# Performance work log

Measured on AMD Instinct MI355X. Metric: run time of the kernel, lower is better.

Reference implementation:

```python
import jax, jax.numpy as jnp
import numpy as np

N, E, H = 100000, 600000, 128
N_MP = 4      # n_mp_down[0]
LN_EPS = 1e-5

def _ln(v, g, b):
    mu = jnp.mean(v, axis=-1, keepdims=True)
    var = jnp.mean((v - mu) ** 2, axis=-1, keepdims=True)
    return (v - mu) * jax.lax.rsqrt(var + LN_EPS) * g + b

def setup_inputs() -> dict:
    key = jax.random.key(0)
    ks = jax.random.split(key, 16)
    s = lambda fan_in: 1.0 / np.sqrt(fan_in)
    inp = {
        "x": jax.random.normal(ks[0], (N, H), jnp.float32),
        "edge_index": jax.random.randint(ks[1], (2, E), 0, N, jnp.int64),
        "edge_attr": jax.random.normal(ks[2], (E, H), jnp.float32),
        "pos": jax.random.uniform(ks[3], (N, 2), jnp.float32),
        "batch": jnp.zeros((N,), jnp.int64),
        # stacked per-iteration params (n_mlp_mp = 2 layers per MLP)
        "edge_w0": jax.random.uniform(ks[4], (N_MP, 3 * H, H), jnp.float32, -s(3 * H), s(3 * H)),
        "edge_b0": jnp.zeros((N_MP, H), jnp.float32),
        "edge_w1": jax.random.uniform(ks[5], (N_MP, H, H), jnp.float32, -s(H), s(H)),
        "edge_b1": jnp.zeros((N_MP, H), jnp.float32),
        "edge_ln_g": jnp.ones((N_MP, H), jnp.float32),
        "edge_ln_b": jnp.zeros((N_MP, H), jnp.float32),
        "node_w0": jax.random.uniform(ks[6], (N_MP, 2 * H, H), jnp.float32, -s(2 * H), s(2 * H)),
        "node_b0": jnp.zeros((N_MP, H), jnp.float32),
        "node_w1": jax.random.uniform(ks[7], (N_MP, H, H), jnp.float32, -s(H), s(H)),
        "node_b1": jnp.zeros((N_MP, H), jnp.float32),
        "node_ln_g": jnp.ones((N_MP, H), jnp.float32),
        "node_ln_b": jnp.zeros((N_MP, H), jnp.float32),
    }
    return inp

def reference(x, edge_index, edge_attr, pos, batch,
              edge_w0, edge_b0, edge_w1, edge_b1, edge_ln_g, edge_ln_b,
              node_w0, node_b0, node_w1, node_b1, node_ln_g, node_ln_b):
    src = edge_index[0]
    tgt = edge_index[1]
    n = x.shape[0]
    # degree for scatter-mean (aggr='mean' at target nodes); zero-degree -> 0
    deg = jax.ops.segment_sum(jnp.ones((edge_attr.shape[0],), x.dtype), tgt, num_segments=n)
    inv_deg = jnp.where(deg > 0, 1.0 / jnp.maximum(deg, 1.0), 0.0)[:, None]
    for i in range(N_MP):
        # edge update MLP with residual + LayerNorm
        e = jnp.concatenate((x[src], x[tgt], edge_attr), axis=1)   # [E, 3H]
        e = jax.nn.elu(e @ edge_w0[i] + edge_b0[i])
        e = e @ edge_w1[i] + edge_b1[i]
        edge_attr = _ln(edge_attr + e, edge_ln_g[i], edge_ln_b[i])
        # scatter-mean edge aggregation -> node update MLP + residual + LN
        agg = jax.ops.segment_sum(edge_attr, tgt, num_segments=n) * inv_deg
        h = jnp.concatenate((x, agg), axis=1)                      # [N, 2H]
        h = jax.nn.elu(h @ node_w0[i] + node_b0[i])
        h = h @ node_w1[i] + node_b1[i]
        x = _ln(x + h, node_ln_g[i], node_ln_b[i])
    return x
```

## Files before the change

kernel.cpp:

```cpp
#include <hip/hip_runtime.h>
#include <hip/hip_bf16.h>

#define N_NODES 100000
#define N_EDGES 600000
#define NMP     4
#define NB_SCAN 391

typedef __attribute__((ext_vector_type(8))) short bf16x8;
typedef __attribute__((ext_vector_type(4))) float f32x4;

#define LGKM0() asm volatile("s_waitcnt lgkmcnt(0)" ::: "memory")

__device__ __forceinline__ short f2bf(float f) {
    union { __hip_bfloat16 h; short s; } u;
    u.h = __float2bfloat16(f);
    return u.s;
}
__device__ __forceinline__ float bf2f(short s) {
    return __uint_as_float(((unsigned int)(unsigned short)s) << 16);
}

__global__ void pack_weights(const float* __restrict__ ew0, const float* __restrict__ ew1,
                             const float* __restrict__ nw0, const float* __restrict__ nw1,
                             short* __restrict__ out) {
    int t = blockIdx.x * blockDim.x + threadIdx.x;
    if (t >= NMP * 14336) return;
    int it = t / 14336;
    int r  = t % 14336;
    const float* W; int obase;
    if (r < 6144)       { W = ew0 + (size_t)it*384*128; obase = 0;     }
    else if (r < 8192)  { W = ew1 + (size_t)it*128*128; obase = 49152; r -= 6144;  }
    else if (r < 12288) { W = nw0 + (size_t)it*256*128; obase = 65536; r -= 8192;  }
    else                { W = nw1 + (size_t)it*128*128; obase = 98304; r -= 12288; }
    int kt   = r >> 9;
    int rem  = r & 511;
    int nt   = rem >> 6;
    int lane = rem & 63;
    short* o = out + (size_t)it*114688 + obase + ((size_t)(kt*8 + nt)*64 + lane)*8;
    int kbase = kt*32 + (lane >> 4)*8;
    int n     = nt*16 + (lane & 15);
    #pragma unroll
    for (int j = 0; j < 8; j++) o[j] = f2bf(W[(size_t)(kbase + j)*128 + n]);
}

__global__ void deg_count(const int* __restrict__ tgt, int* __restrict__ deg) {
    int e = blockIdx.x * blockDim.x + threadIdx.x;
    if (e < N_EDGES) atomicAdd(&deg[tgt[e]], 1);
}

__global__ void scan_reduce(const int* __restrict__ deg, int* __restrict__ bsum) {
    __shared__ int sh[256];
    int i = blockIdx.x * 256 + threadIdx.x;
    sh[threadIdx.x] = (i < N_NODES) ? deg[i] : 0;
    __syncthreads();
    for (int d = 128; d > 0; d >>= 1) {
        if (threadIdx.x < d) sh[threadIdx.x] += sh[threadIdx.x + d];
        __syncthreads();
    }
    if (threadIdx.x == 0) bsum[blockIdx.x] = sh[0];
}

__global__ void scan_top(const int* __restrict__ bsum, int* __restrict__ bbase,
                         int* __restrict__ off) {
    if (threadIdx.x == 0 && blockIdx.x == 0) {
        int run = 0;
        for (int b = 0; b < NB_SCAN; b++) { bbase[b] = run; run += bsum[b]; }
        off[N_NODES] = run;
    }
}

__global__ void scan_apply(const int* __restrict__ deg, const int* __restrict__ bbase,
                           int* __restrict__ off, int* __restrict__ cursor) {
    __shared__ int sh[256];
    int i = blockIdx.x * 256 + threadIdx.x;
    int v = (i < N_NODES) ? deg[i] : 0;
    sh[threadIdx.x] = v;
    __syncthreads();
    int acc = v;
    for (int d = 1; d < 256; d <<= 1) {
        int t = (threadIdx.x >= d) ? sh[threadIdx.x - d] : 0;
        __syncthreads();
        acc += t;
        sh[threadIdx.x] = acc;
        __syncthreads();
    }
    if (i < N_NODES) {
        int o = bbase[blockIdx.x] + acc - v;
        off[i] = o;
        cursor[i] = o;
    }
}

__global__ void fill_csr(const int* __restrict__ tgt, int* __restrict__ cursor,
                         int* __restrict__ elist) {
    int e = blockIdx.x * blockDim.x + threadIdx.x;
    if (e < N_EDGES) {
        int p = atomicAdd(&cursor[tgt[e]], 1);
        elist[p] = e;
    }
}

__global__ void build_perm(const int* __restrict__ srcI, const int* __restrict__ tgtI,
                           const int* __restrict__ elist,
                           int* __restrict__ psrc, int* __restrict__ ptgt) {
    int k = blockIdx.x * blockDim.x + threadIdx.x;
    if (k < N_EDGES) {
        int e = elist[k];
        psrc[k] = srcI[e];
        ptgt[k] = tgtI[e];
    }
}

__global__ __launch_bounds__(256)
void xform_kernel(const float* __restrict__ x_in,
                  short* __restrict__ P, short* __restrict__ Q,
                  const short* __restrict__ w0p) {
    __shared__ __align__(16) short outt[4][16][140];
    const int tid  = threadIdx.x;
    const int wave = tid >> 6, lane = tid & 63;
    const int l15  = lane & 15, lg = lane >> 4;
    const long long nbase = (long long)blockIdx.x * 64 + wave * 16;
    long long arow = nbase + l15;
    if (arow >= N_NODES) arow = N_NODES - 1;

    f32x4 accP[8] = {}, accQ[8] = {};
    const bf16x8* w0f = (const bf16x8*)w0p;
    #pragma unroll
    for (int kt = 0; kt < 4; kt++) {
        const float* ap = x_in + arow*128 + kt*32 + lg*8;
        float4 f0 = *(const float4*)ap;
        float4 f1 = *(const float4*)(ap + 4);
        bf16x8 af;
        af[0]=f2bf(f0.x); af[1]=f2bf(f0.y); af[2]=f2bf(f0.z); af[3]=f2bf(f0.w);
        af[4]=f2bf(f1.x); af[5]=f2bf(f1.y); af[6]=f2bf(f1.z); af[7]=f2bf(f1.w);
        #pragma unroll
        for (int nt = 0; nt < 8; nt++) {
            accP[nt] = __builtin_amdgcn_mfma_f32_16x16x32_bf16(af, w0f[(size_t)(kt*8 + nt)*64 + lane], accP[nt], 0, 0, 0);
            accQ[nt] = __builtin_amdgcn_mfma_f32_16x16x32_bf16(af, w0f[(size_t)((kt+4)*8 + nt)*64 + lane], accQ[nt], 0, 0, 0);
        }
    }
    #pragma unroll
    for (int nt = 0; nt < 8; nt++) {
        int col = nt*16 + l15;
        #pragma unroll
        for (int j = 0; j < 4; j++)
            outt[wave][lg*4 + j][col] = f2bf(accP[nt][j]);
    }
    LGKM0();
    #pragma unroll
    for (int k = 0; k < 4; k++) {
        int row = k*4 + (lane >> 4);
        long long nrow = nbase + row;
        bf16x8 vv = *(const bf16x8*)&outt[wave][row][l15*8];
        if (nrow < N_NODES)
            *(bf16x8*)&P[nrow*128 + l15*8] = vv;
    }
    LGKM0();
    #pragma unroll
    for (int nt = 0; nt < 8; nt++) {
        int col = nt*16 + l15;
        #pragma unroll
        for (int j = 0; j < 4; j++)
            outt[wave][lg*4 + j][col] = f2bf(accQ[nt][j]);
    }
    LGKM0();
    #pragma unroll
    for (int k = 0; k < 4; k++) {
        int row = k*4 + (lane >> 4);
        long long nrow = nbase + row;
        bf16x8 vv = *(const bf16x8*)&outt[wave][row][l15*8];
        if (nrow < N_NODES)
            *(bf16x8*)&Q[nrow*128 + l15*8] = vv;
    }
}

template<bool EAF32>
__global__ __launch_bounds__(512)
void edge_kernel(const short* __restrict__ P,
                 const short* __restrict__ Q,
                 const void* __restrict__ ea_in_v,
                 short* __restrict__ ea_out,
                 const int* __restrict__ psrc,
                 const int* __restrict__ ptgt,
                 const int* __restrict__ elist,
                 const short* __restrict__ w0p,
                 const float* __restrict__ b0,
                 const float* __restrict__ b1,
                 const float* __restrict__ lng,
                 const float* __restrict__ lnb) {
    __shared__ __align__(16) short w1lds[16384];
    __shared__ __align__(16) short pq[8][16][140];
    const int tid  = threadIdx.x;
    const int wave = tid >> 6, lane = tid & 63;
    const int l15  = lane & 15, lg = lane >> 4;
    const long long ebase = (long long)blockIdx.x * 128 + wave * 16;
    const long long arow  = ebase + l15;
    const long long arc   = arow < N_EDGES ? arow : (N_EDGES - 1);
    const float* eaf = (const float*)ea_in_v;
    const short* eab = (const short*)ea_in_v;
    const bf16x8* w0c = (const bf16x8*)(w0p + 32768);

    const short* w1src = w0p + 49152;
    bf16x8 wtmp[4];
    #pragma unroll
    for (int it = 0; it < 4; it++)
        wtmp[it] = *(const bf16x8*)(w1src + it*4096 + tid*8);

    {
        const int c8 = (lane & 7) * 16;
        #pragma unroll
        for (int pass = 0; pass < 2; pass++) {
            int rr = (lane >> 3) + pass * 8;
            long long e = ebase + rr;
            if (e >= N_EDGES) e = N_EDGES - 1;
            long long s = psrc[e], t = ptgt[e];
            bf16x8 p0 = *(const bf16x8*)(P + s*128 + c8);
            bf16x8 p1 = *(const bf16x8*)(P + s*128 + c8 + 8);
            bf16x8 q0 = *(const bf16x8*)(Q + t*128 + c8);
            bf16x8 q1 = *(const bf16x8*)(Q + t*128 + c8 + 8);
            bf16x8 u0, u1;
            #pragma unroll
            for (int k = 0; k < 8; k++) {
                u0[k] = f2bf(bf2f(p0[k]) + bf2f(q0[k]));
                u1[k] = f2bf(bf2f(p1[k]) + bf2f(q1[k]));
            }
            *(bf16x8*)&pq[wave][rr][c8]     = u0;
            *(bf16x8*)&pq[wave][rr][c8 + 8] = u1;
        }
    }

    bf16x8 eafrag[4];
    #pragma unroll
    for (int kt = 0; kt < 4; kt++) {
        if (EAF32) {
            long long orig = elist[arc];
            const float* ap = eaf + orig*128 + kt*32 + lg*8;
            float4 f0 = *(const float4*)ap;
            float4 f1 = *(const float4*)(ap + 4);
            bf16x8 af;
            af[0]=f2bf(f0.x); af[1]=f2bf(f0.y); af[2]=f2bf(f0.z); af[3]=f2bf(f0.w);
            af[4]=f2bf(f1.x); af[5]=f2bf(f1.y); af[6]=f2bf(f1.z); af[7]=f2bf(f1.w);
            eafrag[kt] = af;
        } else {
            eafrag[kt] = *(const bf16x8*)(eab + arc*128 + kt*32 + lg*8);
        }
    }

    #pragma unroll
    for (int it = 0; it < 4; it++)
        *(bf16x8*)&w1lds[it*4096 + tid*8] = wtmp[it];
    __syncthreads();

    f32x4 acc[8] = {};
    #pragma unroll
    for (int kt = 0; kt < 4; kt++) {
        #pragma unroll
        for (int nt = 0; nt < 8; nt++) {
            bf16x8 bfr = w0c[(size_t)(kt*8 + nt)*64 + lane];
            acc[nt] = __builtin_amdgcn_mfma_f32_16x16x32_bf16(eafrag[kt], bfr, acc[nt], 0, 0, 0);
        }
    }

    #pragma unroll
    for (int nt = 0; nt < 8; nt++) {
        int col = nt*16 + l15;
        float bb = b0[col];
        #pragma unroll
        for (int j = 0; j < 4; j++) {
            int r = lg*4 + j;
            float v = acc[nt][j] + bb + bf2f(pq[wave][r][col]);
            v = v > 0.f ? v : (__expf(v) - 1.f);
            pq[wave][r][col] = f2bf(v);
        }
    }
    LGKM0();

    f32x4 acc2[8] = {};
    #pragma unroll
    for (int kt = 0; kt < 4; kt++) {
        bf16x8 af = *(const bf16x8*)&pq[wave][l15][kt*32 + lg*8];
        #pragma unroll
        for (int nt = 0; nt < 8; nt++) {
            bf16x8 bfr = *(const bf16x8*)&w1lds[((kt*8 + nt)*64 + lane)*8];
            acc2[nt] = __builtin_amdgcn_mfma_f32_16x16x32_bf16(af, bfr, acc2[nt], 0, 0, 0);
        }
    }
    LGKM0();

    #pragma unroll
    for (int kt = 0; kt < 4; kt++)
        *(bf16x8*)&pq[wave][l15][kt*32 + lg*8] = eafrag[kt];
    LGKM0();

    float t[8][4];
    #pragma unroll
    for (int nt = 0; nt < 8; nt++) {
        int col = nt*16 + l15;
        float bb = b1[col];
        #pragma unroll
        for (int j = 0; j < 4; j++) {
            int r = lg*4 + j;
            t[nt][j] = acc2[nt][j] + bb + bf2f(pq[wave][r][col]);
        }
    }
    LGKM0();

    #pragma unroll
    for (int j = 0; j < 4; j++) {
        float s = 0.f;
        #pragma unroll
        for (int nt = 0; nt < 8; nt++) s += t[nt][j];
        #pragma unroll
        for (int m = 1; m < 16; m <<= 1) s += __shfl_xor(s, m);
        float mean = s * (1.0f / 128.0f);
        float s2 = 0.f;
        #pragma unroll
        for (int nt = 0; nt < 8; nt++) { float d = t[nt][j] - mean; s2 += d*d; }
        #pragma unroll
        for (int m = 1; m < 16; m <<= 1) s2 += __shfl_xor(s2, m);
        float rstd = rsqrtf(s2 * (1.0f / 128.0f) + 1e-5f);
        int r = lg*4 + j;
        #pragma unroll
        for (int nt = 0; nt < 8; nt++) {
            int col = nt*16 + l15;
            pq[wave][r][col] = f2bf((t[nt][j] - mean) * rstd * lng[col] + lnb[col]);
        }
    }
    LGKM0();

    #pragma unroll
    for (int k = 0; k < 4; k++) {
        int row = k*4 + (lane >> 4);
        long long erow = ebase + row;
        bf16x8 vv = *(const bf16x8*)&pq[wave][row][l15*8];
        if (erow < N_EDGES)
            *(bf16x8*)&ea_out[erow*128 + l15*8] = vv;
    }
}

__global__ __launch_bounds__(256)
void agg_kernel(const short* __restrict__ ea,
                const int* __restrict__ off,
                short* __restrict__ aggb) {
    const int wid  = (blockIdx.x * 256 + threadIdx.x) >> 6;
    const int lane = threadIdx.x & 63;
    if (wid >= N_NODES) return;
    const int o0 = off[wid], o1 = off[wid + 1];
    float s0 = 0.f, s1 = 0.f;
    for (int i = o0; i < o1; i++) {
        unsigned int v = *(const unsigned int*)(ea + (long long)i*128 + lane*2);
        s0 += __uint_as_float(v << 16);
        s1 += __uint_as_float(v & 0xFFFF0000u);
    }
    float inv = (o1 > o0) ? 1.f / (float)(o1 - o0) : 0.f;
    short2 w;
    w.x = f2bf(s0 * inv);
    w.y = f2bf(s1 * inv);
    *(short2*)(aggb + (long long)wid*128 + lane*2) = w;
}

template<bool XF32IN, bool XF32OUT, bool MAKEPQ>
__global__ __launch_bounds__(256)
void node_kernel(const float* __restrict__ xf_in,
                 const short* __restrict__ xb_in,
                 float* __restrict__ xf_out,
                 short* __restrict__ xb_out,
                 const short* __restrict__ aggb,
                 const short* __restrict__ w0p,
                 const short* __restrict__ w1p,
                 const short* __restrict__ wnext,
                 short* __restrict__ P,
                 short* __restrict__ Q,
                 const float* __restrict__ b0,
                 const float* __restrict__ b1,
                 const float* __restrict__ lng,
                 const float* __restrict__ lnb) {
    __shared__ __align__(16) short hid[4][16][140];
    __shared__ __align__(16) short outt[4][16][140];
    const int tid  = threadIdx.x;
    const int wave = tid >> 6, lane = tid & 63;
    const int l15  = lane & 15, lg = lane >> 4;
    const long long nbase = (long long)blockIdx.x * 64 + wave * 16;
    long long arow = nbase + l15;
    if (arow >= N_NODES) arow = N_NODES - 1;

    f32x4 acc[8] = {};
    const bf16x8* w0f = (const bf16x8*)w0p;
    #pragma unroll
    for (int kt = 0; kt < 8; kt++) {
        int k0 = kt*32 + lg*8;
        bf16x8 af;
        if (k0 < 128) {
            if (XF32IN) {
                const float* ap = xf_in + arow*128 + k0;
                float4 f0 = *(const float4*)ap;
                float4 f1 = *(const float4*)(ap + 4);
                af[0]=f2bf(f0.x); af[1]=f2bf(f0.y); af[2]=f2bf(f0.z); af[3]=f2bf(f0.w);
                af[4]=f2bf(f1.x); af[5]=f2bf(f1.y); af[6]=f2bf(f1.z); af[7]=f2bf(f1.w);
            } else {
                af = *(const bf16x8*)(xb_in + arow*128 + k0);
            }
        } else {
            af = *(const bf16x8*)(aggb + arow*128 + (k0 - 128));
        }
        #pragma unroll
        for (int nt = 0; nt < 8; nt++) {
            bf16x8 bfr = w0f[(size_t)(kt*8 + nt)*64 + lane];
            acc[nt] = __builtin_amdgcn_mfma_f32_16x16x32_bf16(af, bfr, acc[nt], 0, 0, 0);
        }
    }
    #pragma unroll
    for (int nt = 0; nt < 8; nt++) {
        int col = nt*16 + l15;
        float bb = b0[col];
        #pragma unroll
        for (int j = 0; j < 4; j++) {
            float v = acc[nt][j] + bb;
            v = v > 0.f ? v : (__expf(v) - 1.f);
            hid[wave][lg*4 + j][col] = f2bf(v);
        }
    }
    LGKM0();

    f32x4 acc2[8] = {};
    const bf16x8* w1f = (const bf16x8*)w1p;
    #pragma unroll
    for (int kt = 0; kt < 4; kt++) {
        bf16x8 af = *(const bf16x8*)&hid[wave][l15][kt*32 + lg*8];
        #pragma unroll
        for (int nt = 0; nt < 8; nt++) {
            bf16x8 bfr = w1f[(size_t)(kt*8 + nt)*64 + lane];
            acc2[nt] = __builtin_amdgcn_mfma_f32_16x16x32_bf16(af, bfr, acc2[nt], 0, 0, 0);
        }
    }
    float t[8][4];
    #pragma unroll
    for (int nt = 0; nt < 8; nt++) {
        int col = nt*16 + l15;
        float bb = b1[col];
        #pragma unroll
        for (int j = 0; j < 4; j++) {
            long long nrow = nbase + lg*4 + j;
            long long nrc  = nrow < N_NODES ? nrow : (N_NODES - 1);
            float res = XF32IN ? xf_in[nrc*128 + col] : bf2f(xb_in[nrc*128 + col]);
            t[nt][j] = acc2[nt][j] + bb + res;
        }
    }
    float xo[8][4];
    #pragma unroll
    for (int j = 0; j < 4; j++) {
        float s = 0.f;
        #pragma unroll
        for (int nt = 0; nt < 8; nt++) s += t[nt][j];
        #pragma unroll
        for (int m = 1; m < 16; m <<= 1) s += __shfl_xor(s, m);
        float mean = s * (1.0f / 128.0f);
        float s2 = 0.f;
        #pragma unroll
        for (int nt = 0; nt < 8; nt++) { float d = t[nt][j] - mean; s2 += d*d; }
        #pragma unroll
        for (int m = 1; m < 16; m <<= 1) s2 += __shfl_xor(s2, m);
        float rstd = rsqrtf(s2 * (1.0f / 128.0f) + 1e-5f);
        long long nrow = nbase + lg*4 + j;
        #pragma unroll
        for (int nt = 0; nt < 8; nt++) {
            int col = nt*16 + l15;
            float v = (t[nt][j] - mean) * rstd * lng[col] + lnb[col];
            xo[nt][j] = v;
            if (XF32OUT && nrow < N_NODES) xf_out[nrow*128 + col] = v;
        }
    }

    if (!XF32OUT || MAKEPQ) {
        LGKM0();
        #pragma unroll
        for (int nt = 0; nt < 8; nt++) {
            int col = nt*16 + l15;
            #pragma unroll
            for (int j = 0; j < 4; j++)
                hid[wave][lg*4 + j][col] = f2bf(xo[nt][j]);
        }
        LGKM0();
    }

    if (!XF32OUT) {
        #pragma unroll
        for (int k = 0; k < 4; k++) {
            int row = k*4 + (lane >> 4);
            long long nrow = nbase + row;
            bf16x8 vv = *(const bf16x8*)&hid[wave][row][l15*8];
            if (nrow < N_NODES)
                *(bf16x8*)&xb_out[nrow*128 + l15*8] = vv;
        }
    }

    if (MAKEPQ) {
        const bf16x8* wn = (const bf16x8*)wnext;
        {
            f32x4 accP[8] = {};
            #pragma unroll
            for (int kt = 0; kt < 4; kt++) {
                bf16x8 af = *(const bf16x8*)&hid[wave][l15][kt*32 + lg*8];
                #pragma unroll
                for (int nt = 0; nt < 8; nt++)
                    accP[nt] = __builtin_amdgcn_mfma_f32_16x16x32_bf16(af, wn[(size_t)(kt*8 + nt)*64 + lane], accP[nt], 0, 0, 0);
            }
            LGKM0();
            #pragma unroll
            for (int nt = 0; nt < 8; nt++) {
                int col = nt*16 + l15;
                #pragma unroll
                for (int j = 0; j < 4; j++)
                    outt[wave][lg*4 + j][col] = f2bf(accP[nt][j]);
            }
            LGKM0();
            #pragma unroll
            for (int k = 0; k < 4; k++) {
                int row = k*4 + (lane >> 4);
                long long nrow = nbase + row;
                bf16x8 vv = *(const bf16x8*)&outt[wave][row][l15*8];
                if (nrow < N_NODES)
                    *(bf16x8*)&P[nrow*128 + l15*8] = vv;
            }
            LGKM0();
        }
        {
            f32x4 accQ[8] = {};
            #pragma unroll
            for (int kt = 0; kt < 4; kt++) {
                bf16x8 af = *(const bf16x8*)&hid[wave][l15][kt*32 + lg*8];
                #pragma unroll
                for (int nt = 0; nt < 8; nt++)
                    accQ[nt] = __builtin_amdgcn_mfma_f32_16x16x32_bf16(af, wn[(size_t)((kt+4)*8 + nt)*64 + lane], accQ[nt], 0, 0, 0);
            }
            LGKM0();
            #pragma unroll
            for (int nt = 0; nt < 8; nt++) {
                int col = nt*16 + l15;
                #pragma unroll
                for (int j = 0; j < 4; j++)
                    outt[wave][lg*4 + j][col] = f2bf(accQ[nt][j]);
            }
            LGKM0();
            #pragma unroll
            for (int k = 0; k < 4; k++) {
                int row = k*4 + (lane >> 4);
                long long nrow = nbase + row;
                bf16x8 vv = *(const bf16x8*)&outt[wave][row][l15*8];
                if (nrow < N_NODES)
                    *(bf16x8*)&Q[nrow*128 + l15*8] = vv;
            }
        }
    }
}

extern "C" void kernel_launch(void* const* d_in, const int* in_sizes, int n_in,
                              void* d_out, int out_size, void* d_ws, size_t ws_size,
                              hipStream_t stream) {
    const float* x_in   = (const float*)d_in[0];
    const int*   eidx   = (const int*)d_in[1];
    const float* ea_in0 = (const float*)d_in[2];
    const float* ew0  = (const float*)d_in[5];
    const float* eb0  = (const float*)d_in[6];
    const float* ew1  = (const float*)d_in[7];
    const float* eb1  = (const float*)d_in[8];
    const float* elng = (const float*)d_in[9];
    const float* elnb = (const float*)d_in[10];
    const float* nw0  = (const float*)d_in[11];
    const float* nb0  = (const float*)d_in[12];
    const float* nw1  = (const float*)d_in[13];
    const float* nb1  = (const float*)d_in[14];
    const float* nlng = (const float*)d_in[15];
    const float* nlnb = (const float*)d_in[16];
    const int* srcI = eidx;
    const int* tgtI = eidx + N_EDGES;

    char* ws = (char*)d_ws;
    size_t o = 0;
    short* ea_bf  = (short*)(ws + o); o += (size_t)N_EDGES * 128 * 2;
    short* Pb     = (short*)(ws + o); o += (size_t)N_NODES * 128 * 2;
    short* Qb     = (short*)(ws + o); o += (size_t)N_NODES * 128 * 2;
    short* aggb   = (short*)(ws + o); o += (size_t)N_NODES * 128 * 2;
    short* xbA    = (short*)(ws + o); o += (size_t)N_NODES * 128 * 2;
    short* xbB    = (short*)(ws + o); o += (size_t)N_NODES * 128 * 2;
    short* wpack  = (short*)(ws + o); o += (size_t)NMP * 114688 * 2;
    int*   deg    = (int*)(ws + o);   o += (size_t)N_NODES * 4;
    int*   offA   = (int*)(ws + o);   o += (size_t)(N_NODES + 1) * 4;
    int*   cursor = (int*)(ws + o);   o += (size_t)N_NODES * 4;
    int*   bsum   = (int*)(ws + o);   o += (size_t)NB_SCAN * 4;
    int*   bbase  = (int*)(ws + o);   o += (size_t)NB_SCAN * 4;
    int*   elist  = (int*)(ws + o);   o += (size_t)N_EDGES * 4;
    int*   psrc   = (int*)(ws + o);   o += (size_t)N_EDGES * 4;
    int*   ptgt   = (int*)(ws + o);   o += (size_t)N_EDGES * 4;
    float* xbuf   = (float*)d_out;

    pack_weights<<<(NMP * 14336 + 255) / 256, 256, 0, stream>>>(ew0, ew1, nw0, nw1, wpack);
    hipMemsetAsync(deg, 0, (size_t)N_NODES * 4, stream);
    deg_count<<<(N_EDGES + 255) / 256, 256, 0, stream>>>(tgtI, deg);
    scan_reduce<<<NB_SCAN, 256, 0, stream>>>(deg, bsum);
    scan_top<<<1, 64, 0, stream>>>(bsum, bbase, offA);
    scan_apply<<<NB_SCAN, 256, 0, stream>>>(deg, bbase, offA, cursor);
    fill_csr<<<(N_EDGES + 255) / 256, 256, 0, stream>>>(tgtI, cursor, elist);
    build_perm<<<(N_EDGES + 255) / 256, 256, 0, stream>>>(srcI, tgtI, elist, psrc, ptgt);

    const int ngrid = (N_NODES + 63) / 64;
    const int egrid = (N_EDGES + 127) / 128;
    xform_kernel<<<ngrid, 256, 0, stream>>>(x_in, Pb, Qb, wpack);

    short* xbin[4]  = {nullptr, xbA, xbB, xbA};
    short* xbout[4] = {xbA, xbB, xbA, nullptr};

    for (int i = 0; i < NMP; i++) {
        const short* wp = wpack + (size_t)i * 114688;
        const short* wnext = wpack + (size_t)(i + 1) * 114688;
        if (i == 0) {
            edge_kernel<true><<<egrid, 512, 0, stream>>>(
                Pb, Qb, (const void*)ea_in0, ea_bf, psrc, ptgt, elist,
                wp + 0,
                eb0 + i * 128, eb1 + i * 128, elng + i * 128, elnb + i * 128);
        } else {
            edge_kernel<false><<<egrid, 512, 0, stream>>>(
                Pb, Qb, (const void*)ea_bf, ea_bf, psrc, ptgt, elist,
                wp + 0,
                eb0 + i * 128, eb1 + i * 128, elng + i * 128, elnb + i * 128);
        }
        agg_kernel<<<(N_NODES * 64 + 255) / 256, 256, 0, stream>>>(ea_bf, offA, aggb);
        if (i == 0) {
            node_kernel<true, false, true><<<ngrid, 256, 0, stream>>>(
                x_in, nullptr, nullptr, xbout[i], aggb,
                wp + 65536, wp + 98304, wnext, Pb, Qb,
                nb0 + i * 128, nb1 + i * 128, nlng + i * 128, nlnb + i * 128);
        } else if (i < NMP - 1) {
            node_kernel<false, false, true><<<ngrid, 256, 0, stream>>>(
                nullptr, xbin[i], nullptr, xbout[i], aggb,
                wp + 65536, wp + 98304, wnext, Pb, Qb,
                nb0 + i * 128, nb1 + i * 128, nlng + i * 128, nlnb + i * 128);
        } else {
            node_kernel<false, true, false><<<ngrid, 256, 0, stream>>>(
                nullptr, xbin[i], xbuf, nullptr, aggb,
                wp + 65536, wp + 98304, wnext, Pb, Qb,
                nb0 + i * 128, nb1 + i * 128, nlng + i * 128, nlnb + i * 128);
        }
    }
}
```

Measured before the change: 1.132 ms.

## Fuse scatter-mean aggregation into node kernel via LDS staging

Removes the separate agg_kernel and computes the per-node mean of sorted edge features inside node_kernel. Each lane of a wave sums 16 columns for one of 8 nodes per pass and writes the bf16 result into the outt shared tile, which then feeds the MFMA A operand. This drops one kernel launch and the write and re-read of the aggregation buffer per iteration. In exchange, each lane does a serial gather over the node's edges with more registers, and per-wave parallelism over the gather is lower than the old one-wave-per-node layout, so load latency may be exposed.

```diff
diff --git a/kernel.cpp b/kernel.cpp
--- a/kernel.cpp
+++ b/kernel.cpp
@@ -338,34 +338,14 @@
     }
 }
 
-__global__ __launch_bounds__(256)
-void agg_kernel(const short* __restrict__ ea,
-                const int* __restrict__ off,
-                short* __restrict__ aggb) {
-    const int wid  = (blockIdx.x * 256 + threadIdx.x) >> 6;
-    const int lane = threadIdx.x & 63;
-    if (wid >= N_NODES) return;
-    const int o0 = off[wid], o1 = off[wid + 1];
-    float s0 = 0.f, s1 = 0.f;
-    for (int i = o0; i < o1; i++) {
-        unsigned int v = *(const unsigned int*)(ea + (long long)i*128 + lane*2);
-        s0 += __uint_as_float(v << 16);
-        s1 += __uint_as_float(v & 0xFFFF0000u);
-    }
-    float inv = (o1 > o0) ? 1.f / (float)(o1 - o0) : 0.f;
-    short2 w;
-    w.x = f2bf(s0 * inv);
-    w.y = f2bf(s1 * inv);
-    *(short2*)(aggb + (long long)wid*128 + lane*2) = w;
-}
-
 template<bool XF32IN, bool XF32OUT, bool MAKEPQ>
 __global__ __launch_bounds__(256)
 void node_kernel(const float* __restrict__ xf_in,
                  const short* __restrict__ xb_in,
                  float* __restrict__ xf_out,
                  short* __restrict__ xb_out,
-                 const short* __restrict__ aggb,
+                 const short* __restrict__ ea,
+                 const int* __restrict__ off,
                  const short* __restrict__ w0p,
                  const short* __restrict__ w1p,
                  const short* __restrict__ wnext,
@@ -384,6 +364,40 @@
     long long arow = nbase + l15;
     if (arow >= N_NODES) arow = N_NODES - 1;
 
+    {
+        const int sub = lane >> 3;
+        const int cb  = (lane & 7) * 16;
+        #pragma unroll
+        for (int pass = 0; pass < 2; pass++) {
+            int nl = pass * 8 + sub;
+            long long n = nbase + nl;
+            if (n >= N_NODES) n = N_NODES - 1;
+            int o0 = off[n], o1 = off[n + 1];
+            float sums[16];
+            #pragma unroll
+            for (int c = 0; c < 16; c++) sums[c] = 0.f;
+            for (int i = o0; i < o1; i++) {
+                bf16x8 v0 = *(const bf16x8*)(ea + (long long)i*128 + cb);
+                bf16x8 v1 = *(const bf16x8*)(ea + (long long)i*128 + cb + 8);
+                #pragma unroll
+                for (int c = 0; c < 8; c++) {
+                    sums[c]     += bf2f(v0[c]);
+                    sums[c + 8] += bf2f(v1[c]);
+                }
+            }
+            float inv = (o1 > o0) ? 1.f / (float)(o1 - o0) : 0.f;
+            bf16x8 wv0, wv1;
+            #pragma unroll
+            for (int c = 0; c < 8; c++) {
+                wv0[c] = f2bf(sums[c] * inv);
+                wv1[c] = f2bf(sums[c + 8] * inv);
+            }
+            *(bf16x8*)&outt[wave][nl][cb]     = wv0;
+            *(bf16x8*)&outt[wave][nl][cb + 8] = wv1;
+        }
+    }
+    LGKM0();
+
     f32x4 acc[8] = {};
     const bf16x8* w0f = (const bf16x8*)w0p;
     #pragma unroll
@@ -401,7 +415,7 @@
                 af = *(const bf16x8*)(xb_in + arow*128 + k0);
             }
         } else {
-            af = *(const bf16x8*)(aggb + arow*128 + (k0 - 128));
+            af = *(const bf16x8*)&outt[wave][l15][k0 - 128];
         }
         #pragma unroll
         for (int nt = 0; nt < 8; nt++) {
@@ -580,7 +594,6 @@
     short* ea_bf  = (short*)(ws + o); o += (size_t)N_EDGES * 128 * 2;
     short* Pb     = (short*)(ws + o); o += (size_t)N_NODES * 128 * 2;
     short* Qb     = (short*)(ws + o); o += (size_t)N_NODES * 128 * 2;
-    short* aggb   = (short*)(ws + o); o += (size_t)N_NODES * 128 * 2;
     short* xbA    = (short*)(ws + o); o += (size_t)N_NODES * 128 * 2;
     short* xbB    = (short*)(ws + o); o += (size_t)N_NODES * 128 * 2;
     short* wpack  = (short*)(ws + o); o += (size_t)NMP * 114688 * 2;
@@ -624,20 +637,19 @@
                 wp + 0,
                 eb0 + i * 128, eb1 + i * 128, elng + i * 128, elnb + i * 128);
         }
-        agg_kernel<<<(N_NODES * 64 + 255) / 256, 256, 0, stream>>>(ea_bf, offA, aggb);
         if (i == 0) {
             node_kernel<true, false, true><<<ngrid, 256, 0, stream>>>(
-                x_in, nullptr, nullptr, xbout[i], aggb,
+                x_in, nullptr, nullptr, xbout[i], ea_bf, offA,
                 wp + 65536, wp + 98304, wnext, Pb, Qb,
                 nb0 + i * 128, nb1 + i * 128, nlng + i * 128, nlnb + i * 128);
         } else if (i < NMP - 1) {
             node_kernel<false, false, true><<<ngrid, 256, 0, stream>>>(
-                nullptr, xbin[i], nullptr, xbout[i], aggb,
+                nullptr, xbin[i], nullptr, xbout[i], ea_bf, offA,
                 wp + 65536, wp + 98304, wnext, Pb, Qb,
                 nb0 + i * 128, nb1 + i * 128, nlng + i * 128, nlnb + i * 128);
         } else {
             node_kernel<false, true, false><<<ngrid, 256, 0, stream>>>(
-                nullptr, xbin[i], xbuf, nullptr, aggb,
+                nullptr, xbin[i], xbuf, nullptr, ea_bf, offA,
                 wp + 65536, wp + 98304, wnext, Pb, Qb,
                 nb0 + i * 128, nb1 + i * 128, nlng + i * 128, nlnb + i * 128);
         }
```

Measured after the change: 1.043 ms, median of 2. -7.9%, faster.
